# Kernel optimization log

Hardware: AMD Instinct MI355X
Metric: run time of the kernel (lower is better)

The kernel has to match this reference:

```python
import jax, jax.numpy as jnp
import numpy as np
from jax import lax

DISCOUNT = 0.99
NORMALIZE = True
EPS = 1e-9


def setup_inputs() -> dict:
    key = jax.random.key(0)
    k1, k2 = jax.random.split(key)
    B, T = 4096, 8192
    rewards = jax.random.normal(k1, (B, T), dtype=jnp.float32)
    done_flags = (jax.random.uniform(k2, (B, T)) < 0.01).astype(jnp.float32)
    return {"rewards": rewards, "done_flags": done_flags}


def _episode_returns(rewards, done_flags):
    # reverse-time recurrence: r_t = rew_t + gamma * r_{t+1} * (1 - done_t)
    rw = jnp.moveaxis(rewards, -1, 0)      # [T, B]
    dn = jnp.moveaxis(done_flags, -1, 0)   # [T, B]

    def step(carry, xs):
        r, d = xs
        ret = r + DISCOUNT * carry * (1.0 - d)
        return ret, ret

    # init carry = 0 makes the last step reduce to returns[-1] = rewards[-1]
    _, rets = lax.scan(step, jnp.zeros_like(rw[0]), (rw, dn), reverse=True)
    returns = jnp.moveaxis(rets, 0, -1)    # [B, T]

    if NORMALIZE:
        # torch: (returns - returns.mean()) / (returns.std(dim=-1) + 1e-9)
        # global mean, per-trajectory std (unbiased, matching torch default)
        std = jnp.std(returns, axis=-1, ddof=1, keepdims=True)
        returns = (returns - jnp.mean(returns)) / (std + EPS)
    return returns


def reference(rewards, done_flags):
    return _episode_returns(rewards, done_flags)
```

## Files before the change

kernel.cpp:

```cpp
#include <hip/hip_runtime.h>
#include <math.h>

#define TLEN  8192
#define BROWS 4096
#define GAMMA 0.99f
#define EPSN  1e-9

__global__ __launch_bounds__(256) void er_scan(const float* __restrict__ rew,
                                               const float* __restrict__ don,
                                               float* __restrict__ out,
                                               double* __restrict__ rowSum,
                                               float* __restrict__ rowInv) {
  const int row = blockIdx.x;
  const int tid = threadIdx.x;
  const size_t base = (size_t)row * TLEN + (size_t)tid * 32;

  float4 rv[8], dv[8];
  float* rw = (float*)rv;
  float* dn = (float*)dv;

  const float4* r4 = (const float4*)(rew + base);
  const float4* d4 = (const float4*)(don + base);
#pragma unroll
  for (int k = 0; k < 8; ++k) rv[k] = r4[k];
#pragma unroll
  for (int k = 0; k < 8; ++k) dv[k] = d4[k];

  float A = 0.f, P = 1.f;
#pragma unroll
  for (int j = 31; j >= 0; --j) {
    const float c = GAMMA - GAMMA * dn[j];
    A = fmaf(c, A, rw[j]);
    P = P * c;
    rw[j] = A;
    dn[j] = P;
  }

  const int lane = tid & 63;
  const int wv   = tid >> 6;
  float sA = A, sP = P;
#pragma unroll
  for (int d = 1; d < 64; d <<= 1) {
    const float tA = __shfl_down(sA, d);
    const float tP = __shfl_down(sP, d);
    if (lane + d < 64) { sA = fmaf(sP, tA, sA); sP *= tP; }
  }

  __shared__ float  wgA[4], wgP[4];
  __shared__ double red[8];
  if (lane == 0) { wgA[wv] = sA; wgP[wv] = sP; }
  __syncthreads();

  float wc = 0.f;
  for (int j = 3; j > wv; --j) wc = fmaf(wgP[j], wc, wgA[j]);

  float eA = __shfl_down(sA, 1);
  float eP = __shfl_down(sP, 1);
  if (lane == 63) { eA = 0.f; eP = 1.f; }
  const float carry = fmaf(eP, wc, eA);

  float fsum = 0.f, fsq = 0.f;
#pragma unroll
  for (int j = 0; j < 32; ++j) {
    const float r = fmaf(dn[j], carry, rw[j]);
    rw[j] = r;
    fsum += r;
    fsq  = fmaf(r, r, fsq);
  }
  float4* o4 = (float4*)(out + base);
#pragma unroll
  for (int k = 0; k < 8; ++k) o4[k] = rv[k];

  double ds = (double)fsum, dq = (double)fsq;
#pragma unroll
  for (int d = 32; d >= 1; d >>= 1) {
    ds += __shfl_down(ds, d);
    dq += __shfl_down(dq, d);
  }
  if (lane == 0) { red[wv] = ds; red[4 + wv] = dq; }
  __syncthreads();
  if (tid == 0) {
    const double s = red[0] + red[1] + red[2] + red[3];
    const double q = red[4] + red[5] + red[6] + red[7];
    rowSum[row] = s;
    double var = (q - s * s / (double)TLEN) / (double)(TLEN - 1);
    if (var < 0.0) var = 0.0;
    rowInv[row] = (float)(1.0 / (sqrt(var) + EPSN));
  }
}

__global__ __launch_bounds__(256) void er_mean(const double* __restrict__ rowSum,
                                               float* __restrict__ meanPtr) {
  const int tid = threadIdx.x;
  double s = 0.0;
  for (int i = tid; i < BROWS; i += 256) s += rowSum[i];
#pragma unroll
  for (int d = 32; d >= 1; d >>= 1) s += __shfl_down(s, d);
  __shared__ double red[4];
  const int lane = tid & 63, wv = tid >> 6;
  if (lane == 0) red[wv] = s;
  __syncthreads();
  if (tid == 0) {
    const double t = red[0] + red[1] + red[2] + red[3];
    *meanPtr = (float)(t / ((double)BROWS * (double)TLEN));
  }
}

__global__ __launch_bounds__(256) void er_norm(float* __restrict__ out,
                                               const float* __restrict__ rowInv,
                                               const float* __restrict__ meanPtr) {
  const int row = blockIdx.x;
  const float mean = *meanPtr;
  const float inv  = rowInv[row];
  float4* o4 = (float4*)(out + (size_t)row * TLEN);
#pragma unroll
  for (int i = threadIdx.x; i < TLEN / 4; i += 256) {
    float4 v = o4[i];
    v.x = (v.x - mean) * inv;
    v.y = (v.y - mean) * inv;
    v.z = (v.z - mean) * inv;
    v.w = (v.w - mean) * inv;
    o4[i] = v;
  }
}

extern "C" void kernel_launch(void* const* d_in, const int* in_sizes, int n_in,
                              void* d_out, int out_size, void* d_ws, size_t ws_size,
                              hipStream_t stream) {
  const float* rew = (const float*)d_in[0];
  const float* don = (const float*)d_in[1];
  float* out = (float*)d_out;

  double* rowSum  = (double*)d_ws;
  float*  rowInv  = (float*)((char*)d_ws + BROWS * 8);
  float*  meanPtr = (float*)((char*)d_ws + BROWS * 8 + BROWS * 4);

  er_scan<<<BROWS, 256, 0, stream>>>(rew, don, out, rowSum, rowInv);
  er_mean<<<1, 256, 0, stream>>>(rowSum, meanPtr);
  er_norm<<<BROWS, 256, 0, stream>>>(out, rowInv, meanPtr);
}
```

Baseline: 361.0 us.

## Tile scan kernel over time with LDS-staged coalesced loads and register prefetch

The scan kernel now walks each row in four 2048-element tiles from the end backwards. Each tile's rewards and done flags are loaded with fully coalesced float4 reads, transposed through padded LDS, and the next tile's loads are issued before the current tile is computed. A tile-to-tile carry chains the scans. The goal is better load coalescing and lower register use than the old per-thread 32-element strided loads, which should raise occupancy and overlap memory with compute. The cost is extra barriers and LDS traffic per tile, plus a serial dependency across tiles.

After: 353.2 us. 1.02x faster.

```diff
diff --git a/kernel.cpp b/kernel.cpp
--- a/kernel.cpp
+++ b/kernel.cpp
@@ -1,77 +1,129 @@
 #include <hip/hip_runtime.h>
 #include <math.h>
 
-#define TLEN  8192
-#define BROWS 4096
-#define GAMMA 0.99f
-#define EPSN  1e-9
+#define TLEN   8192
+#define BROWS  4096
+#define NT     256
+#define TILE   2048
+#define CHUNK  8
+#define NTILES (TLEN / TILE)
+#define GAMMA  0.99f
+#define EPSN   1e-9
 
-__global__ __launch_bounds__(256) void er_scan(const float* __restrict__ rew,
-                                               const float* __restrict__ don,
-                                               float* __restrict__ out,
-                                               double* __restrict__ rowSum,
-                                               float* __restrict__ rowInv) {
-  const int row = blockIdx.x;
-  const int tid = threadIdx.x;
-  const size_t base = (size_t)row * TLEN + (size_t)tid * 32;
+__device__ __forceinline__ void stash(float* lds, int e0, float4 v) {
+  const int w = e0 + (e0 >> 3);
+  lds[w + 0] = v.x;
+  lds[w + 1] = v.y;
+  lds[w + 2] = v.z;
+  lds[w + 3] = v.w;
+}
 
-  float4 rv[8], dv[8];
-  float* rw = (float*)rv;
-  float* dn = (float*)dv;
+__global__ __launch_bounds__(NT) void er_scan(const float* __restrict__ rew,
+                                              const float* __restrict__ don,
+                                              float* __restrict__ out,
+                                              double* __restrict__ rowSum,
+                                              float* __restrict__ rowInv) {
+  __shared__ float  ldsR[TILE + TILE / 8];
+  __shared__ float  ldsD[TILE + TILE / 8];
+  __shared__ float  wgA[4], wgP[4];
+  __shared__ double red[8];
 
-  const float4* r4 = (const float4*)(rew + base);
-  const float4* d4 = (const float4*)(don + base);
+  const int row  = blockIdx.x;
+  const int tid  = threadIdx.x;
+  const int lane = tid & 63;
+  const int wv   = tid >> 6;
+  const size_t rbase = (size_t)row * TLEN;
+
+  const float4* gr = (const float4*)(rew + rbase);
+  const float4* gd = (const float4*)(don + rbase);
+
+  float4 pr0, pr1, pd0, pd1;
+  {
+    const int f = (NTILES - 1) * (TILE / 4);
+    pr0 = gr[f + tid];      pr1 = gr[f + NT + tid];
+    pd0 = gd[f + tid];      pd1 = gd[f + NT + tid];
+  }
+  stash(ldsR, 4 * tid, pr0);  stash(ldsR, 1024 + 4 * tid, pr1);
+  stash(ldsD, 4 * tid, pd0);  stash(ldsD, 1024 + 4 * tid, pd1);
+  __syncthreads();
+
+  double accS = 0.0, accQ = 0.0;
+  float  tc = 0.f;
+
+  for (int k = NTILES - 1; k >= 0; --k) {
+    const bool more = (k > 0);
+    if (more) {
+      const int f = (k - 1) * (TILE / 4);
+      pr0 = gr[f + tid];    pr1 = gr[f + NT + tid];
+      pd0 = gd[f + tid];    pd1 = gd[f + NT + tid];
+    }
+
+    float rv[CHUNK], cv[CHUNK];
+    const int wbase = 9 * tid;
 #pragma unroll
-  for (int k = 0; k < 8; ++k) rv[k] = r4[k];
+    for (int j = 0; j < CHUNK; ++j) rv[j] = ldsR[wbase + j];
 #pragma unroll
-  for (int k = 0; k < 8; ++k) dv[k] = d4[k];
+    for (int j = 0; j < CHUNK; ++j) cv[j] = GAMMA - GAMMA * ldsD[wbase + j];
 
-  float A = 0.f, P = 1.f;
+    float A = 0.f, P = 1.f;
 #pragma unroll
-  for (int j = 31; j >= 0; --j) {
-    const float c = GAMMA - GAMMA * dn[j];
-    A = fmaf(c, A, rw[j]);
-    P = P * c;
-    rw[j] = A;
-    dn[j] = P;
+    for (int j = CHUNK - 1; j >= 0; --j) {
+      A = fmaf(cv[j], A, rv[j]);
+      P *= cv[j];
+      rv[j] = A;
+      cv[j] = P;
+    }
+
+    float sA = A, sP = P;
+#pragma unroll
+    for (int d = 1; d < 64; d <<= 1) {
+      const float tA = __shfl_down(sA, d);
+      const float tP = __shfl_down(sP, d);
+      if (lane + d < 64) { sA = fmaf(sP, tA, sA); sP *= tP; }
+    }
+    if (lane == 0) { wgA[wv] = sA; wgP[wv] = sP; }
+    __syncthreads();
+
+    float wc = tc;
+#pragma unroll
+    for (int j = 3; j >= 1; --j) {
+      const float nw = fmaf(wgP[j], wc, wgA[j]);
+      wc = (j > wv) ? nw : wc;
+    }
+    float tcn = tc;
+#pragma unroll
+    for (int j = 3; j >= 0; --j) tcn = fmaf(wgP[j], tcn, wgA[j]);
+
+    float eA = __shfl_down(sA, 1);
+    float eP = __shfl_down(sP, 1);
+    if (lane == 63) { eA = 0.f; eP = 1.f; }
+    const float carry = fmaf(eP, wc, eA);
+
+    if (more) {
+      stash(ldsR, 4 * tid, pr0);  stash(ldsR, 1024 + 4 * tid, pr1);
+      stash(ldsD, 4 * tid, pd0);  stash(ldsD, 1024 + 4 * tid, pd1);
+    }
+
+    float fsum = 0.f, fsq = 0.f;
+    float o[CHUNK];
+#pragma unroll
+    for (int j = 0; j < CHUNK; ++j) {
+      const float r = fmaf(cv[j], carry, rv[j]);
+      o[j] = r;
+      fsum += r;
+      fsq  = fmaf(r, r, fsq);
+    }
+    float4* go = (float4*)(out + rbase + (size_t)k * TILE + (size_t)tid * CHUNK);
+    go[0] = make_float4(o[0], o[1], o[2], o[3]);
+    go[1] = make_float4(o[4], o[5], o[6], o[7]);
+    accS += (double)fsum;
+    accQ += (double)fsq;
+    tc = tcn;
+
+    if (more) __syncthreads();
   }
 
-  const int lane = tid & 63;
-  const int wv   = tid >> 6;
-  float sA = A, sP = P;
-#pragma unroll
-  for (int d = 1; d < 64; d <<= 1) {
-    const float tA = __shfl_down(sA, d);
-    const float tP = __shfl_down(sP, d);
-    if (lane + d < 64) { sA = fmaf(sP, tA, sA); sP *= tP; }
-  }
-
-  __shared__ float  wgA[4], wgP[4];
-  __shared__ double red[8];
-  if (lane == 0) { wgA[wv] = sA; wgP[wv] = sP; }
-  __syncthreads();
-
-  float wc = 0.f;
-  for (int j = 3; j > wv; --j) wc = fmaf(wgP[j], wc, wgA[j]);
-
-  float eA = __shfl_down(sA, 1);
-  float eP = __shfl_down(sP, 1);
-  if (lane == 63) { eA = 0.f; eP = 1.f; }
-  const float carry = fmaf(eP, wc, eA);
-
-  float fsum = 0.f, fsq = 0.f;
-#pragma unroll
-  for (int j = 0; j < 32; ++j) {
-    const float r = fmaf(dn[j], carry, rw[j]);
-    rw[j] = r;
-    fsum += r;
-    fsq  = fmaf(r, r, fsq);
-  }
-  float4* o4 = (float4*)(out + base);
-#pragma unroll
-  for (int k = 0; k < 8; ++k) o4[k] = rv[k];
-
-  double ds = (double)fsum, dq = (double)fsq;
+  double ds = accS, dq = accQ;
 #pragma unroll
   for (int d = 32; d >= 1; d >>= 1) {
     ds += __shfl_down(ds, d);
@@ -135,7 +187,7 @@
   float*  rowInv  = (float*)((char*)d_ws + BROWS * 8);
   float*  meanPtr = (float*)((char*)d_ws + BROWS * 8 + BROWS * 4);
 
-  er_scan<<<BROWS, 256, 0, stream>>>(rew, don, out, rowSum, rowInv);
+  er_scan<<<BROWS, NT, 0, stream>>>(rew, don, out, rowSum, rowInv);
   er_mean<<<1, 256, 0, stream>>>(rowSum, meanPtr);
   er_norm<<<BROWS, 256, 0, stream>>>(out, rowInv, meanPtr);
 }
```

## Split row scan into segment-level affine passes with algebraic statistics

Applied to the files above, without the earlier changes.

Each 8192-long row is split into 8 segments of 1024, handled by their own blocks. A first pass computes each segment's affine composition (A, P) along with sums of a, p, a², ap and p². A single-block middle kernel chains the segment carries, then derives row sums, variance, per-row inverse std and the global mean from those moments. A second pass recomputes the local scan from the inputs and writes the normalized output directly, which removes the separate normalize pass that re-read and re-wrote the output. This buys more parallelism with lighter per-thread state, at the cost of reading the inputs twice and computing the statistics in float32 from moments, which may lose precision.

After: 371.0 us. 2.7% more time.

```diff
diff --git a/kernel.cpp b/kernel.cpp
--- a/kernel.cpp
+++ b/kernel.cpp
@@ -3,41 +3,50 @@
 
 #define TLEN  8192
 #define BROWS 4096
+#define SEG   1024
+#define NSEG  8
+#define NBLK  (BROWS * NSEG)
+#define NT    256
+#define CH    4
 #define GAMMA 0.99f
 #define EPSN  1e-9
 
-__global__ __launch_bounds__(256) void er_scan(const float* __restrict__ rew,
-                                               const float* __restrict__ don,
-                                               float* __restrict__ out,
-                                               double* __restrict__ rowSum,
-                                               float* __restrict__ rowInv) {
-  const int row = blockIdx.x;
-  const int tid = threadIdx.x;
-  const size_t base = (size_t)row * TLEN + (size_t)tid * 32;
-
-  float4 rv[8], dv[8];
-  float* rw = (float*)rv;
-  float* dn = (float*)dv;
-
-  const float4* r4 = (const float4*)(rew + base);
-  const float4* d4 = (const float4*)(don + base);
-#pragma unroll
-  for (int k = 0; k < 8; ++k) rv[k] = r4[k];
-#pragma unroll
-  for (int k = 0; k < 8; ++k) dv[k] = d4[k];
-
+__global__ __launch_bounds__(NT) void er_segA(const float* __restrict__ rew,
+                                              const float* __restrict__ don,
+                                              float* __restrict__ fA,  float* __restrict__ fP,
+                                              float* __restrict__ fSa, float* __restrict__ fSp,
+                                              float* __restrict__ fSaa,float* __restrict__ fSap,
+                                              float* __restrict__ fSpp) {
+  const int blk  = blockIdx.x;
+  const int tid  = threadIdx.x;
+  const int lane = tid & 63, wv = tid >> 6;
+  const size_t base = (size_t)blk * SEG + (size_t)tid * CH;
+
+  const float4 rv = *(const float4*)(rew + base);
+  const float4 dv = *(const float4*)(don + base);
+
+  float a[CH], p[CH];
   float A = 0.f, P = 1.f;
-#pragma unroll
-  for (int j = 31; j >= 0; --j) {
-    const float c = GAMMA - GAMMA * dn[j];
-    A = fmaf(c, A, rw[j]);
-    P = P * c;
-    rw[j] = A;
-    dn[j] = P;
-  }
-
-  const int lane = tid & 63;
-  const int wv   = tid >> 6;
+  {
+    const float r[CH] = {rv.x, rv.y, rv.z, rv.w};
+    const float d[CH] = {dv.x, dv.y, dv.z, dv.w};
+#pragma unroll
+    for (int j = CH - 1; j >= 0; --j) {
+      const float c = GAMMA - GAMMA * d[j];
+      A = fmaf(c, A, r[j]);
+      P *= c;
+      a[j] = A; p[j] = P;
+    }
+  }
+  float sa = 0.f, sp = 0.f, saa = 0.f, sap = 0.f, spp = 0.f;
+#pragma unroll
+  for (int j = 0; j < CH; ++j) {
+    sa += a[j]; sp += p[j];
+    saa = fmaf(a[j], a[j], saa);
+    sap = fmaf(a[j], p[j], sap);
+    spp = fmaf(p[j], p[j], spp);
+  }
+
   float sA = A, sP = P;
 #pragma unroll
   for (int d = 1; d < 64; d <<= 1) {
@@ -45,83 +54,173 @@
     const float tP = __shfl_down(sP, d);
     if (lane + d < 64) { sA = fmaf(sP, tA, sA); sP *= tP; }
   }
-
-  __shared__ float  wgA[4], wgP[4];
-  __shared__ double red[8];
+  __shared__ float wgA[4], wgP[4];
+  __shared__ float red[20];
   if (lane == 0) { wgA[wv] = sA; wgP[wv] = sP; }
   __syncthreads();
 
-  float wc = 0.f;
-  for (int j = 3; j > wv; --j) wc = fmaf(wgP[j], wc, wgA[j]);
-
+  float vA = 0.f, vP = 1.f;
+#pragma unroll
+  for (int j = 3; j >= 1; --j) {
+    const float nA = fmaf(wgP[j], vA, wgA[j]);
+    const float nP = vP * wgP[j];
+    if (j > wv) { vA = nA; vP = nP; }
+  }
   float eA = __shfl_down(sA, 1);
   float eP = __shfl_down(sP, 1);
   if (lane == 63) { eA = 0.f; eP = 1.f; }
-  const float carry = fmaf(eP, wc, eA);
-
-  float fsum = 0.f, fsq = 0.f;
-#pragma unroll
-  for (int j = 0; j < 32; ++j) {
-    const float r = fmaf(dn[j], carry, rw[j]);
-    rw[j] = r;
-    fsum += r;
-    fsq  = fmaf(r, r, fsq);
-  }
-  float4* o4 = (float4*)(out + base);
-#pragma unroll
-  for (int k = 0; k < 8; ++k) o4[k] = rv[k];
-
-  double ds = (double)fsum, dq = (double)fsq;
+  const float EA = fmaf(eP, vA, eA);
+  const float EP = eP * vP;
+
+  float ca  = fmaf(EA, sp, sa);
+  float cp  = EP * sp;
+  float caa = fmaf(EA, fmaf(2.f, sap, EA * spp), saa);
+  float cap = EP * fmaf(EA, spp, sap);
+  float cpp = EP * EP * spp;
+
 #pragma unroll
   for (int d = 32; d >= 1; d >>= 1) {
-    ds += __shfl_down(ds, d);
-    dq += __shfl_down(dq, d);
-  }
-  if (lane == 0) { red[wv] = ds; red[4 + wv] = dq; }
+    ca  += __shfl_down(ca, d);
+    cp  += __shfl_down(cp, d);
+    caa += __shfl_down(caa, d);
+    cap += __shfl_down(cap, d);
+    cpp += __shfl_down(cpp, d);
+  }
+  if (lane == 0) {
+    red[wv] = ca; red[4 + wv] = cp; red[8 + wv] = caa;
+    red[12 + wv] = cap; red[16 + wv] = cpp;
+  }
   __syncthreads();
   if (tid == 0) {
-    const double s = red[0] + red[1] + red[2] + red[3];
-    const double q = red[4] + red[5] + red[6] + red[7];
-    rowSum[row] = s;
-    double var = (q - s * s / (double)TLEN) / (double)(TLEN - 1);
+    fSa[blk]  = red[0]  + red[1]  + red[2]  + red[3];
+    fSp[blk]  = red[4]  + red[5]  + red[6]  + red[7];
+    fSaa[blk] = red[8]  + red[9]  + red[10] + red[11];
+    fSap[blk] = red[12] + red[13] + red[14] + red[15];
+    fSpp[blk] = red[16] + red[17] + red[18] + red[19];
+    float gA = 0.f, gP = 1.f;
+#pragma unroll
+    for (int j = 3; j >= 0; --j) { gA = fmaf(wgP[j], gA, wgA[j]); gP *= wgP[j]; }
+    fA[blk] = gA; fP[blk] = gP;
+  }
+}
+
+__global__ __launch_bounds__(256) void er_mid(const float* __restrict__ fA,  const float* __restrict__ fP,
+                                              const float* __restrict__ fSa, const float* __restrict__ fSp,
+                                              const float* __restrict__ fSaa,const float* __restrict__ fSap,
+                                              const float* __restrict__ fSpp,
+                                              float* __restrict__ cArr,
+                                              float* __restrict__ rowInv,
+                                              float* __restrict__ meanPtr) {
+  const int tid = threadIdx.x;
+  double tsum = 0.0;
+  for (int i = 0; i < BROWS / 256; ++i) {
+    const int r  = tid + 256 * i;
+    const int b0 = r * NSEG;
+    float A[NSEG], P[NSEG], Sa[NSEG], Sp[NSEG], Saa[NSEG], Sap[NSEG], Spp[NSEG];
+#pragma unroll
+    for (int h = 0; h < 2; ++h) {
+      *(float4*)(A   + 4*h) = ((const float4*)(fA   + b0))[h];
+      *(float4*)(P   + 4*h) = ((const float4*)(fP   + b0))[h];
+      *(float4*)(Sa  + 4*h) = ((const float4*)(fSa  + b0))[h];
+      *(float4*)(Sp  + 4*h) = ((const float4*)(fSp  + b0))[h];
+      *(float4*)(Saa + 4*h) = ((const float4*)(fSaa + b0))[h];
+      *(float4*)(Sap + 4*h) = ((const float4*)(fSap + b0))[h];
+      *(float4*)(Spp + 4*h) = ((const float4*)(fSpp + b0))[h];
+    }
+    float c[NSEG];
+    float v = 0.f;
+#pragma unroll
+    for (int s = NSEG - 1; s >= 0; --s) { c[s] = v; v = fmaf(P[s], v, A[s]); }
+
+    double rs = 0.0, rq = 0.0;
+#pragma unroll
+    for (int s = 0; s < NSEG; ++s) {
+      rs += (double)fmaf(Sp[s], c[s], Sa[s]);
+      rq += (double)fmaf(c[s], fmaf(2.f, Sap[s], c[s] * Spp[s]), Saa[s]);
+    }
+#pragma unroll
+    for (int h = 0; h < 2; ++h)
+      ((float4*)(cArr + b0))[h] = *(const float4*)(c + 4*h);
+
+    double var = (rq - rs * rs / (double)TLEN) / (double)(TLEN - 1);
     if (var < 0.0) var = 0.0;
-    rowInv[row] = (float)(1.0 / (sqrt(var) + EPSN));
-  }
-}
-
-__global__ __launch_bounds__(256) void er_mean(const double* __restrict__ rowSum,
-                                               float* __restrict__ meanPtr) {
-  const int tid = threadIdx.x;
-  double s = 0.0;
-  for (int i = tid; i < BROWS; i += 256) s += rowSum[i];
-#pragma unroll
-  for (int d = 32; d >= 1; d >>= 1) s += __shfl_down(s, d);
-  __shared__ double red[4];
+    rowInv[r] = (float)(1.0 / (sqrt(var) + EPSN));
+    tsum += rs;
+  }
+#pragma unroll
+  for (int d = 32; d >= 1; d >>= 1) tsum += __shfl_down(tsum, d);
+  __shared__ double dred[4];
   const int lane = tid & 63, wv = tid >> 6;
-  if (lane == 0) red[wv] = s;
+  if (lane == 0) dred[wv] = tsum;
   __syncthreads();
   if (tid == 0) {
-    const double t = red[0] + red[1] + red[2] + red[3];
+    const double t = dred[0] + dred[1] + dred[2] + dred[3];
     *meanPtr = (float)(t / ((double)BROWS * (double)TLEN));
   }
 }
 
-__global__ __launch_bounds__(256) void er_norm(float* __restrict__ out,
-                                               const float* __restrict__ rowInv,
-                                               const float* __restrict__ meanPtr) {
-  const int row = blockIdx.x;
-  const float mean = *meanPtr;
-  const float inv  = rowInv[row];
-  float4* o4 = (float4*)(out + (size_t)row * TLEN);
-#pragma unroll
-  for (int i = threadIdx.x; i < TLEN / 4; i += 256) {
-    float4 v = o4[i];
-    v.x = (v.x - mean) * inv;
-    v.y = (v.y - mean) * inv;
-    v.z = (v.z - mean) * inv;
-    v.w = (v.w - mean) * inv;
-    o4[i] = v;
-  }
+__global__ __launch_bounds__(NT) void er_segB(const float* __restrict__ rew,
+                                              const float* __restrict__ don,
+                                              const float* __restrict__ cArr,
+                                              const float* __restrict__ rowInv,
+                                              const float* __restrict__ meanPtr,
+                                              float* __restrict__ out) {
+  const int blk  = blockIdx.x;
+  const int tid  = threadIdx.x;
+  const int lane = tid & 63, wv = tid >> 6;
+  const size_t base = (size_t)blk * SEG + (size_t)tid * CH;
+
+  const float4 rv = *(const float4*)(rew + base);
+  const float4 dv = *(const float4*)(don + base);
+
+  float a[CH], p[CH];
+  float A = 0.f, P = 1.f;
+  {
+    const float r[CH] = {rv.x, rv.y, rv.z, rv.w};
+    const float d[CH] = {dv.x, dv.y, dv.z, dv.w};
+#pragma unroll
+    for (int j = CH - 1; j >= 0; --j) {
+      const float c = GAMMA - GAMMA * d[j];
+      A = fmaf(c, A, r[j]);
+      P *= c;
+      a[j] = A; p[j] = P;
+    }
+  }
+  float sA = A, sP = P;
+#pragma unroll
+  for (int d = 1; d < 64; d <<= 1) {
+    const float tA = __shfl_down(sA, d);
+    const float tP = __shfl_down(sP, d);
+    if (lane + d < 64) { sA = fmaf(sP, tA, sA); sP *= tP; }
+  }
+  __shared__ float wgA[4], wgP[4];
+  if (lane == 0) { wgA[wv] = sA; wgP[wv] = sP; }
+  __syncthreads();
+
+  float vA = 0.f, vP = 1.f;
+#pragma unroll
+  for (int j = 3; j >= 1; --j) {
+    const float nA = fmaf(wgP[j], vA, wgA[j]);
+    const float nP = vP * wgP[j];
+    if (j > wv) { vA = nA; vP = nP; }
+  }
+  float eA = __shfl_down(sA, 1);
+  float eP = __shfl_down(sP, 1);
+  if (lane == 63) { eA = 0.f; eP = 1.f; }
+  const float EA = fmaf(eP, vA, eA);
+  const float EP = eP * vP;
+
+  const float cs    = cArr[blk];
+  const float carry = fmaf(EP, cs, EA);
+  const float mean  = *meanPtr;
+  const float inv   = rowInv[blk >> 3];
+
+  float4 o;
+  o.x = (fmaf(p[0], carry, a[0]) - mean) * inv;
+  o.y = (fmaf(p[1], carry, a[1]) - mean) * inv;
+  o.z = (fmaf(p[2], carry, a[2]) - mean) * inv;
+  o.w = (fmaf(p[3], carry, a[3]) - mean) * inv;
+  *(float4*)(out + base) = o;
 }
 
 extern "C" void kernel_launch(void* const* d_in, const int* in_sizes, int n_in,
@@ -131,11 +230,19 @@
   const float* don = (const float*)d_in[1];
   float* out = (float*)d_out;
 
-  double* rowSum  = (double*)d_ws;
-  float*  rowInv  = (float*)((char*)d_ws + BROWS * 8);
-  float*  meanPtr = (float*)((char*)d_ws + BROWS * 8 + BROWS * 4);
-
-  er_scan<<<BROWS, 256, 0, stream>>>(rew, don, out, rowSum, rowInv);
-  er_mean<<<1, 256, 0, stream>>>(rowSum, meanPtr);
-  er_norm<<<BROWS, 256, 0, stream>>>(out, rowInv, meanPtr);
-}
+  float* w      = (float*)d_ws;
+  float* fA     = w + 0 * NBLK;
+  float* fP     = w + 1 * NBLK;
+  float* fSa    = w + 2 * NBLK;
+  float* fSp    = w + 3 * NBLK;
+  float* fSaa   = w + 4 * NBLK;
+  float* fSap   = w + 5 * NBLK;
+  float* fSpp   = w + 6 * NBLK;
+  float* cArr   = w + 7 * NBLK;
+  float* rowInv = w + 8 * NBLK;
+  float* meanPtr= w + 8 * NBLK + BROWS;
+
+  er_segA<<<NBLK, NT, 0, stream>>>(rew, don, fA, fP, fSa, fSp, fSaa, fSap, fSpp);
+  er_mid<<<1, 256, 0, stream>>>(fA, fP, fSa, fSp, fSaa, fSap, fSpp, cArr, rowInv, meanPtr);
+  er_segB<<<NBLK, NT, 0, stream>>>(rew, don, cArr, rowInv, meanPtr, out);
+}
```
